# Performance work log

Measured on AMD Instinct MI355X. Metric: run time of the kernel, lower is better.

The kernel has to match this reference:

```python
import jax, jax.numpy as jnp
import numpy as np

N_NODES = 10000
N_EDGES = 320000
IN_DIM = 512
HID = 64
H0 = 8
OUT = 64
H1 = 1
NEG_SLOPE = 0.2


def gat_layer(h, src, dst, W, attn_l, attn_r, n_nodes, activation=None):
    # h: (N, F_in); W: (F_in, H*D); attn_l/attn_r: (H, D)
    H, D = attn_l.shape
    feat = (h @ W).reshape(n_nodes, H, D)            # (N, H, D)
    el = jnp.einsum('nhd,hd->nh', feat, attn_l)      # (N, H)
    er = jnp.einsum('nhd,hd->nh', feat, attn_r)      # (N, H)
    e = jax.nn.leaky_relu(el[src] + er[dst], NEG_SLOPE)  # (E, H)
    # edge softmax over incoming edges of each destination node
    m = jax.ops.segment_max(e, dst, num_segments=n_nodes)   # (N, H), -inf for isolated
    m = jnp.where(jnp.isfinite(m), m, 0.0)
    ex = jnp.exp(e - m[dst])                         # (E, H)
    s = jax.ops.segment_sum(ex, dst, num_segments=n_nodes)  # (N, H)
    alpha = ex / s[dst]                              # (E, H)
    # weighted aggregation: out[dst] += alpha * feat[src]
    out = jax.ops.segment_sum(alpha[:, :, None] * feat[src], dst,
                              num_segments=n_nodes)  # (N, H, D)
    if activation is not None:
        out = activation(out)
    return out


def setup_inputs() -> dict:
    key = jax.random.key(0)
    ks = jax.random.split(key, 9)
    h = jax.random.normal(ks[0], (N_NODES, IN_DIM), dtype=jnp.float32)
    src = jax.random.randint(ks[1], (N_EDGES,), 0, N_NODES, dtype=jnp.int32)
    dst = jax.random.randint(ks[2], (N_EDGES,), 0, N_NODES, dtype=jnp.int32)
    W1 = jax.random.normal(ks[3], (IN_DIM, H0 * HID), dtype=jnp.float32) / np.sqrt(IN_DIM)
    attn_l1 = jax.random.normal(ks[4], (H0, HID), dtype=jnp.float32) / np.sqrt(HID)
    attn_r1 = jax.random.normal(ks[5], (H0, HID), dtype=jnp.float32) / np.sqrt(HID)
    W2 = jax.random.normal(ks[6], (H0 * HID, H1 * OUT), dtype=jnp.float32) / np.sqrt(H0 * HID)
    attn_l2 = jax.random.normal(ks[7], (H1, OUT), dtype=jnp.float32) / np.sqrt(OUT)
    attn_r2 = jax.random.normal(ks[8], (H1, OUT), dtype=jnp.float32) / np.sqrt(OUT)
    return {"h": h, "src": src, "dst": dst, "W1": W1, "attn_l1": attn_l1,
            "attn_r1": attn_r1, "W2": W2, "attn_l2": attn_l2, "attn_r2": attn_r2}


def reference(h, src, dst, W1, attn_l1, attn_r1, W2, attn_l2, attn_r2):
    # layer 1: elu activation, concat heads (flatten)
    x = gat_layer(h, src, dst, W1, attn_l1, attn_r1, N_NODES, activation=jax.nn.elu)
    x = x.reshape(N_NODES, H0 * HID)
    # layer 2: no activation, mean over heads
    x = gat_layer(x, src, dst, W2, attn_l2, attn_r2, N_NODES, activation=None)
    return x.mean(axis=1)  # (N, OUT)
```

## Files before the change

kernel.cpp:

```cpp
#include <hip/hip_runtime.h>
#include <hip/hip_bf16.h>
#include <math.h>

typedef unsigned int u32;
typedef unsigned short ushort;

constexpr int N_NODES = 10000;
constexpr int N_EDGES = 320000;
constexpr float NEG_SLOPE = 0.2f;

typedef __attribute__((ext_vector_type(8))) _Float16 half8;
typedef __attribute__((ext_vector_type(4))) float f32x4;
typedef __attribute__((ext_vector_type(16))) float f32x16;

__device__ __forceinline__ float lrelu(float x) { return x > 0.f ? x : NEG_SLOPE * x; }
__device__ __forceinline__ float elu(float x)   { return x > 0.f ? x : (expf(x) - 1.f); }

__device__ __forceinline__ ushort f2h(float x) {
    _Float16 h = (_Float16)x;
    return __builtin_bit_cast(ushort, h);
}
__device__ __forceinline__ float h2f(ushort u) {
    return (float)__builtin_bit_cast(_Float16, u);
}

__device__ __forceinline__ void gload16(const void* g, void* l) {
    __builtin_amdgcn_global_load_lds(
        (__attribute__((address_space(1))) void*)g,
        (__attribute__((address_space(3))) void*)l, 16, 0, 0);
}

constexpr int NB_HIST  = (N_EDGES + 255) / 256;
constexpr int NB_SPLIT = (N_NODES * 512 / 4) / 256;

__global__ void prep1_kernel(const float4* __restrict__ h4,
                             ushort* __restrict__ xh,
                             const int* __restrict__ dst, int* __restrict__ counts,
                             int* __restrict__ rank) {
    const int b = blockIdx.x;
    if (b < NB_HIST) {
        const int i = b * 256 + threadIdx.x;
        if (i < N_EDGES) rank[i] = atomicAdd(&counts[dst[i]], 1);
    } else {
        const int i = (b - NB_HIST) * 256 + threadIdx.x;
        const float4 v = h4[i];
        *(ushort4*)&xh[i * 4] = make_ushort4(f2h(v.x), f2h(v.y), f2h(v.z), f2h(v.w));
    }
}

constexpr int NB_T1   = 64;
constexpr int NB_T2   = 8;
constexpr int NB_WLR2 = 2;

__global__ void prep2_kernel(const float* __restrict__ W1,
                             ushort* __restrict__ w1t,
                             const float* __restrict__ W2,
                             ushort* __restrict__ w2t,
                             const float* __restrict__ al2, const float* __restrict__ ar2,
                             float* __restrict__ wl2, float* __restrict__ wr2,
                             const int* __restrict__ counts, int* __restrict__ offs) {
    __shared__ float smem[64][65];
    const int b = blockIdx.x;
    if (b < NB_T1 + NB_T2) {
        const bool isW1 = b < NB_T1;
        const float* W = isW1 ? W1 : W2;
        ushort* wt = isW1 ? w1t : w2t;
        const int N  = isW1 ? 512 : 64;
        const int t  = isW1 ? b : (b - NB_T1);
        const int ti = isW1 ? (t & 7) : t;
        const int tj = isW1 ? (t >> 3) : 0;
        const int c  = threadIdx.x & 63;
        const int r0 = threadIdx.x >> 6;
#pragma unroll
        for (int p = 0; p < 16; p++) {
            const int r = p * 4 + r0;
            smem[r][c] = W[(size_t)(ti * 64 + r) * N + tj * 64 + c];
        }
        __syncthreads();
#pragma unroll
        for (int p = 0; p < 16; p++) {
            const int rr = p * 4 + r0;
            wt[(size_t)(tj * 64 + rr) * 512 + ti * 64 + c] = f2h(smem[c][rr]);
        }
    } else if (b < NB_T1 + NB_T2 + NB_WLR2) {
        const int k = (b - NB_T1 - NB_T2) * 256 + threadIdx.x;
        float sl = 0.f, sr = 0.f;
#pragma unroll 8
        for (int d = 0; d < 64; d++) {
            const float w = W2[(size_t)k * 64 + d];
            sl += w * al2[d];
            sr += w * ar2[d];
        }
        wl2[k] = sl;
        wr2[k] = sr;
    } else {
        __shared__ int wsum[4];
        const int tid = threadIdx.x;
        const int lane = tid & 63, wave = tid >> 6;
        const int base = tid * 40;
        int v[40];
        int s = 0;
#pragma unroll
        for (int i = 0; i < 40; i++) {
            v[i] = (base + i < N_NODES) ? counts[base + i] : 0;
            s += v[i];
        }
        int ps = s;
#pragma unroll
        for (int o = 1; o < 64; o <<= 1) {
            const int t = __shfl_up(ps, o);
            if (lane >= o) ps += t;
        }
        if (lane == 63) wsum[wave] = ps;
        __syncthreads();
        if (tid < 4) {
            int t = wsum[tid];
#pragma unroll
            for (int o = 1; o < 4; o <<= 1) {
                const int u = __shfl_up(t, o);
                if (tid >= o) t += u;
            }
            wsum[tid] = t;
        }
        __syncthreads();
        const int wbase = (wave > 0) ? wsum[wave - 1] : 0;
        int run = wbase + ps - s;
#pragma unroll
        for (int i = 0; i < 40; i++) {
            if (base + i < N_NODES) offs[base + i + 1] = run + v[i];
            run += v[i];
        }
        if (tid == 0) offs[0] = 0;
    }
}

constexpr int NB_GEMM1 = ((N_NODES + 63) / 64) * 4;
constexpr int NB_SCAT  = (N_EDGES + 255) / 256;

__global__ __launch_bounds__(256) void gemm1_scatter_kernel(
    const ushort* __restrict__ A, const ushort* __restrict__ B,
    ushort* __restrict__ Cout, int M,
    const float* __restrict__ attn_l, const float* __restrict__ attn_r,
    float* __restrict__ elp, float* __restrict__ erp,
    const int* __restrict__ src, const int* __restrict__ dst,
    const int* __restrict__ rank, const int* __restrict__ offs,
    int* __restrict__ srcs) {
    constexpr int BM = 64, BN = 128, BK = 32, K = 512, N = 512;

    if ((int)blockIdx.x >= NB_GEMM1) {
        const int i = ((int)blockIdx.x - NB_GEMM1) * 256 + threadIdx.x;
        if (i < N_EDGES) srcs[offs[dst[i]] + rank[i]] = src[i];
        return;
    }

    __shared__ __align__(16) ushort sA[BM * BK];
    __shared__ __align__(16) ushort sB[BN * BK];

    const int tid = threadIdx.x;
    const int wave = tid >> 6, lane = tid & 63;
    const int m0 = ((int)blockIdx.x >> 2) * BM, n0 = ((int)blockIdx.x & 3) * BN;
    const int wm = wave >> 1, wn = wave & 1;
    const int l31 = lane & 31, lh = lane >> 5;

    const int fb = wave * 1024 + lane * 16;

    int arow = m0 + (fb >> 6);
    if (arow > M - 1) arow = M - 1;
    const size_t abyte = (size_t)arow * (K * 2) + (fb & 63);
    size_t bbyte[2];
#pragma unroll
    for (int r = 0; r < 2; r++) {
        const int f = fb + r * 4096;
        bbyte[r] = (size_t)(n0 + (f >> 6)) * (K * 2) + (f & 63);
    }

    f32x16 acc[2] = {};

    for (int k0 = 0; k0 < K; k0 += BK) {
        __syncthreads();
        const size_t kb = (size_t)k0 * 2;
        gload16((const char*)A + abyte + kb, (char*)sA + fb);
#pragma unroll
        for (int r = 0; r < 2; r++) {
            const int f = fb + r * 4096;
            gload16((const char*)B + bbyte[r] + kb, (char*)sB + f);
        }
        __syncthreads();

#pragma unroll
        for (int ks = 0; ks < 2; ks++) {
            const int koff = ks * 16 + lh * 8;
            const half8 ah = *(const half8*)&sA[(wm * 32 + l31) * BK + koff];
#pragma unroll
            for (int ni = 0; ni < 2; ni++) {
                const half8 bh = *(const half8*)&sB[(wn * 64 + ni * 32 + l31) * BK + koff];
                acc[ni] = __builtin_amdgcn_mfma_f32_32x32x16_f16(ah, bh, acc[ni], 0, 0, 0);
            }
        }
    }

#pragma unroll
    for (int reg = 0; reg < 16; reg++) {
        const int grow = m0 + wm * 32 + (reg & 3) + 8 * (reg >> 2) + 4 * lh;
        if (grow < M) {
#pragma unroll
            for (int ni = 0; ni < 2; ni++) {
                const int gcol = n0 + wn * 64 + ni * 32 + l31;
                Cout[(size_t)grow * N + gcol] = f2h(acc[ni][reg]);
            }
        }
    }

    const int head = (n0 + wn * 64) >> 6;
    float alv[2], arv[2];
#pragma unroll
    for (int ni = 0; ni < 2; ni++) {
        alv[ni] = attn_l[head * 64 + ni * 32 + l31];
        arv[ni] = attn_r[head * 64 + ni * 32 + l31];
    }
#pragma unroll
    for (int reg = 0; reg < 16; reg++) {
        float pl = acc[0][reg] * alv[0] + acc[1][reg] * alv[1];
        float pr = acc[0][reg] * arv[0] + acc[1][reg] * arv[1];
#pragma unroll
        for (int o = 1; o < 32; o <<= 1) {
            pl += __shfl_xor(pl, o);
            pr += __shfl_xor(pr, o);
        }
        const int grow = m0 + wm * 32 + (reg & 3) + 8 * (reg >> 2) + 4 * lh;
        if (l31 == 0 && grow < M) {
            elp[grow * 8 + head] = pl;
            erp[grow * 8 + head] = pr;
        }
    }
}

__global__ __launch_bounds__(256) void gemm2_kernel(
    const ushort* __restrict__ A, const ushort* __restrict__ B,
    ushort* __restrict__ Cout, int M) {
    constexpr int BM = 64, BN = 64, BK = 32, K = 512, N = 64;
    constexpr int WM = 32, WN = 32, MT_M = 2, MT_N = 2;

    __shared__ __align__(16) ushort sA[BM * BK];
    __shared__ __align__(16) ushort sB[BN * BK];

    const int tid = threadIdx.x;
    const int wave = tid >> 6, lane = tid & 63;
    const int m0 = blockIdx.x * BM;
    const int wm = wave >> 1, wn = wave & 1;
    const int quad = lane >> 4, l15 = lane & 15;

    const int fb = wave * 1024 + lane * 16;

    int arow = m0 + (fb >> 6);
    if (arow > M - 1) arow = M - 1;
    const size_t abyte = (size_t)arow * (K * 2) + (fb & 63);
    const size_t bbyte = (size_t)(fb >> 6) * (K * 2) + (fb & 63);

    f32x4 acc[MT_M][MT_N] = {};

    for (int k0 = 0; k0 < K; k0 += BK) {
        __syncthreads();
        const size_t kb = (size_t)k0 * 2;
        gload16((const char*)A + abyte + kb, (char*)sA + fb);
        gload16((const char*)B + bbyte + kb, (char*)sB + fb);
        __syncthreads();

        half8 ah[MT_M], bh[MT_N];
#pragma unroll
        for (int mi = 0; mi < MT_M; mi++) {
            const int row = wm * WM + mi * 16 + l15;
            ah[mi] = *(const half8*)&sA[row * BK + quad * 8];
        }
#pragma unroll
        for (int ni = 0; ni < MT_N; ni++) {
            const int row = wn * WN + ni * 16 + l15;
            bh[ni] = *(const half8*)&sB[row * BK + quad * 8];
        }
#pragma unroll
        for (int mi = 0; mi < MT_M; mi++)
#pragma unroll
            for (int ni = 0; ni < MT_N; ni++)
                acc[mi][ni] = __builtin_amdgcn_mfma_f32_16x16x32_f16(ah[mi], bh[ni], acc[mi][ni], 0, 0, 0);
    }

#pragma unroll
    for (int mi = 0; mi < MT_M; mi++) {
#pragma unroll
        for (int r = 0; r < 4; r++) {
            const int grow = m0 + wm * WM + mi * 16 + quad * 4 + r;
            if (grow < M) {
#pragma unroll
                for (int ni = 0; ni < MT_N; ni++) {
                    const int gcol = wn * WN + ni * 16 + l15;
                    Cout[(size_t)grow * N + gcol] = f2h(acc[mi][ni][r]);
                }
            }
        }
    }
}

__global__ __launch_bounds__(256) void agg1_kernel(
    const ushort* __restrict__ feat, const float* __restrict__ el,
    const float* __restrict__ er, const int* __restrict__ offs,
    const int* __restrict__ srcs, ushort* __restrict__ xh,
    const float* __restrict__ wl2, const float* __restrict__ wr2,
    float* __restrict__ el2, float* __restrict__ er2) {
    const int tid = threadIdx.x;
    const int wave = tid >> 6, lane = tid & 63;
    const int node = blockIdx.x * 4 + wave;
    const int start = offs[node];
    const int deg = offs[node + 1] - start;
    const int d0 = lane * 8;
    const int myh = lane >> 3;

    if (deg == 0) {
        const ushort4 z = make_ushort4(0, 0, 0, 0);
        *(ushort4*)&xh[(size_t)node * 512 + d0] = z;
        *(ushort4*)&xh[(size_t)node * 512 + d0 + 4] = z;
        if (lane == 0) { el2[node] = 0.f; er2[node] = 0.f; }
        return;
    }

    const float4 ea = *(const float4*)&er[node * 8];
    const float4 eb = *(const float4*)&er[node * 8 + 4];
    const float er_my = (myh & 4) ? ((myh & 2) ? ((myh & 1) ? eb.w : eb.z)
                                              : ((myh & 1) ? eb.y : eb.x))
                                  : ((myh & 2) ? ((myh & 1) ? ea.w : ea.z)
                                              : ((myh & 1) ? ea.y : ea.x));

    float acc[8];
#pragma unroll
    for (int i = 0; i < 8; i++) acc[i] = 0.f;
    float ws = 0.f;

    for (int base = 0; base < deg; base += 64) {
        const int has = min(64, deg - base);
        const int s = srcs[start + base + min(lane, has - 1)];
        int j = 0;
        for (; j + 8 <= has; j += 8) {
            int sq[8];
#pragma unroll
            for (int q = 0; q < 8; q++) sq[q] = __shfl(s, j + q);
            float eq[8];
#pragma unroll
            for (int q = 0; q < 8; q++) eq[q] = el[sq[q] * 8 + myh];
            half8 uq[8];
#pragma unroll
            for (int q = 0; q < 8; q++)
                uq[q] = *(const half8*)&feat[(size_t)sq[q] * 512 + d0];
            float wq[8];
#pragma unroll
            for (int q = 0; q < 8; q++) wq[q] = __expf(lrelu(eq[q] + er_my));
#pragma unroll
            for (int q = 0; q < 8; q++) {
#pragma unroll
                for (int i = 0; i < 8; i++)
                    acc[i] += wq[q] * (float)uq[q][i];
                ws += wq[q];
            }
        }
        for (; j < has; j++) {
            const int sj = __shfl(s, j);
            const float w = __expf(lrelu(el[sj * 8 + myh] + er_my));
            const half8 u = *(const half8*)&feat[(size_t)sj * 512 + d0];
#pragma unroll
            for (int i = 0; i < 8; i++)
                acc[i] += w * (float)u[i];
            ws += w;
        }
    }

    const float inv = 1.f / ws;
    float o[8];
#pragma unroll
    for (int i = 0; i < 8; i++) o[i] = elu(acc[i] * inv);

    const float4 wla = *(const float4*)&wl2[d0];
    const float4 wlb = *(const float4*)&wl2[d0 + 4];
    const float4 wra = *(const float4*)&wr2[d0];
    const float4 wrb = *(const float4*)&wr2[d0 + 4];
    float pl = o[0] * wla.x + o[1] * wla.y + o[2] * wla.z + o[3] * wla.w
             + o[4] * wlb.x + o[5] * wlb.y + o[6] * wlb.z + o[7] * wlb.w;
    float pr = o[0] * wra.x + o[1] * wra.y + o[2] * wra.z + o[3] * wra.w
             + o[4] * wrb.x + o[5] * wrb.y + o[6] * wrb.z + o[7] * wrb.w;
#pragma unroll
    for (int off = 32; off > 0; off >>= 1) {
        pl += __shfl_xor(pl, off);
        pr += __shfl_xor(pr, off);
    }
    if (lane == 0) { el2[node] = pl; er2[node] = pr; }

    ushort hh[8];
#pragma unroll
    for (int i = 0; i < 8; i++) hh[i] = f2h(o[i]);
    *(ushort4*)&xh[(size_t)node * 512 + d0]     = make_ushort4(hh[0], hh[1], hh[2], hh[3]);
    *(ushort4*)&xh[(size_t)node * 512 + d0 + 4] = make_ushort4(hh[4], hh[5], hh[6], hh[7]);
}

__global__ __launch_bounds__(256) void agg2_kernel(
    const ushort* __restrict__ feat, const float* __restrict__ el,
    const float* __restrict__ er, const int* __restrict__ offs,
    const int* __restrict__ srcs, float* __restrict__ out) {
    const int tid = threadIdx.x;
    const int wave = tid >> 6, lane = tid & 63;
    const int node = blockIdx.x * 4 + wave;
    const int start = offs[node];
    const int deg = offs[node + 1] - start;
    if (deg == 0) { out[(size_t)node * 64 + lane] = 0.f; return; }
    const float ern = er[node];

    float acc = 0.f, ws = 0.f;
    for (int base = 0; base < deg; base += 64) {
        const int has = min(64, deg - base);
        const int s = srcs[start + base + min(lane, has - 1)];
        const float w = __expf(lrelu(el[s] + ern));
        int j = 0;
        for (; j + 8 <= has; j += 8) {
            float aq[8]; int sq[8];
#pragma unroll
            for (int q = 0; q < 8; q++) { aq[q] = __shfl(w, j + q); sq[q] = __shfl(s, j + q); }
            ushort fq[8];
#pragma unroll
            for (int q = 0; q < 8; q++) fq[q] = feat[(size_t)sq[q] * 64 + lane];
#pragma unroll
            for (int q = 0; q < 8; q++) { acc += aq[q] * h2f(fq[q]); ws += aq[q]; }
        }
        for (; j < has; j++) {
            const float a = __shfl(w, j);
            const int sj = __shfl(s, j);
            acc += a * h2f(feat[(size_t)sj * 64 + lane]);
            ws += a;
        }
    }
    out[(size_t)node * 64 + lane] = acc / ws;
}

extern "C" void kernel_launch(void* const* d_in, const int* in_sizes, int n_in,
                              void* d_out, int out_size, void* d_ws, size_t ws_size,
                              hipStream_t stream) {
    const float* h   = (const float*)d_in[0];
    const int*   src = (const int*)d_in[1];
    const int*   dst = (const int*)d_in[2];
    const float* W1  = (const float*)d_in[3];
    const float* al1 = (const float*)d_in[4];
    const float* ar1 = (const float*)d_in[5];
    const float* W2  = (const float*)d_in[6];
    const float* al2 = (const float*)d_in[7];
    const float* ar2 = (const float*)d_in[8];
    float* out = (float*)d_out;

    char* p = (char*)d_ws;
    ushort* feat1 = (ushort*)p; p += (size_t)N_NODES * 512 * 2;
    ushort* feat2 = (ushort*)p; p += (size_t)N_NODES * 64 * 2;
    float* el1   = (float*)p;  p += (size_t)N_NODES * 8 * 4;
    float* er1   = (float*)p;  p += (size_t)N_NODES * 8 * 4;
    float* el2   = (float*)p;  p += (size_t)N_NODES * 4;
    float* er2   = (float*)p;  p += (size_t)N_NODES * 4;
    ushort* xh   = (ushort*)p; p += (size_t)N_NODES * 512 * 2;
    ushort* w1t  = (ushort*)p; p += (size_t)512 * 512 * 2;
    ushort* w2t  = (ushort*)p; p += (size_t)64 * 512 * 2;
    float* wl2   = (float*)p;  p += (size_t)512 * 4;
    float* wr2   = (float*)p;  p += (size_t)512 * 4;
    int* counts  = (int*)p;    p += (size_t)N_NODES * 4;
    int* offs    = (int*)p;    p += (size_t)10004 * 4;
    int* rank    = (int*)p;    p += (size_t)N_EDGES * 4;
    int* srcs    = (int*)p;    p += (size_t)N_EDGES * 4;

    hipMemsetAsync(counts, 0, (size_t)N_NODES * 4, stream);

    prep1_kernel<<<NB_HIST + NB_SPLIT, 256, 0, stream>>>(
        (const float4*)h, xh, dst, counts, rank);

    prep2_kernel<<<NB_T1 + NB_T2 + NB_WLR2 + 1, 256, 0, stream>>>(
        W1, w1t, W2, w2t, al2, ar2, wl2, wr2, counts, offs);

    gemm1_scatter_kernel<<<NB_GEMM1 + NB_SCAT, 256, 0, stream>>>(
        xh, w1t, feat1, N_NODES, al1, ar1, el1, er1,
        src, dst, rank, offs, srcs);

    agg1_kernel<<<N_NODES / 4, 256, 0, stream>>>(
        feat1, el1, er1, offs, srcs, xh, wl2, wr2, el2, er2);

    gemm2_kernel<<<(N_NODES + 63) / 64, 256, 0, stream>>>(
        xh, w2t, feat2, N_NODES);

    agg2_kernel<<<N_NODES / 4, 256, 0, stream>>>(feat2, el2, er2, offs, srcs, out);
}
```

Before: 194.7 us.

## Double-buffer and swizzle LDS in both GEMMs, merge weight prep into first kernel

Both GEMM kernels now use BK=64 with double-buffered LDS tiles, prefetching the next k-tile via global_load_lds while computing the current one. An XOR swizzle on the LDS layout is meant to avoid bank conflicts. gemm2 halves BM to launch more blocks. The weight transpose and wl2/wr2 work moves into prep1 so that the single-block scan kernel runs alone, overlapping the prep work with the histogram and cast. The prefetch relies on the trailing __syncthreads per iteration to ensure the loads have completed.

```diff
diff --git a/kernel.cpp b/kernel.cpp
--- a/kernel.cpp
+++ b/kernel.cpp
@@ -31,42 +31,32 @@
 }
 
 constexpr int NB_HIST  = (N_EDGES + 255) / 256;
+constexpr int NB_T1    = 64;
+constexpr int NB_T2    = 8;
+constexpr int NB_WLR2  = 2;
+constexpr int NB_PRE   = NB_HIST + NB_T1 + NB_T2 + NB_WLR2;
 constexpr int NB_SPLIT = (N_NODES * 512 / 4) / 256;
 
 __global__ void prep1_kernel(const float4* __restrict__ h4,
                              ushort* __restrict__ xh,
                              const int* __restrict__ dst, int* __restrict__ counts,
-                             int* __restrict__ rank) {
+                             int* __restrict__ rank,
+                             const float* __restrict__ W1, ushort* __restrict__ w1t,
+                             const float* __restrict__ W2, ushort* __restrict__ w2t,
+                             const float* __restrict__ al2, const float* __restrict__ ar2,
+                             float* __restrict__ wl2, float* __restrict__ wr2) {
+    __shared__ float smem[64][65];
     const int b = blockIdx.x;
     if (b < NB_HIST) {
         const int i = b * 256 + threadIdx.x;
         if (i < N_EDGES) rank[i] = atomicAdd(&counts[dst[i]], 1);
-    } else {
-        const int i = (b - NB_HIST) * 256 + threadIdx.x;
-        const float4 v = h4[i];
-        *(ushort4*)&xh[i * 4] = make_ushort4(f2h(v.x), f2h(v.y), f2h(v.z), f2h(v.w));
-    }
-}
-
-constexpr int NB_T1   = 64;
-constexpr int NB_T2   = 8;
-constexpr int NB_WLR2 = 2;
-
-__global__ void prep2_kernel(const float* __restrict__ W1,
-                             ushort* __restrict__ w1t,
-                             const float* __restrict__ W2,
-                             ushort* __restrict__ w2t,
-                             const float* __restrict__ al2, const float* __restrict__ ar2,
-                             float* __restrict__ wl2, float* __restrict__ wr2,
-                             const int* __restrict__ counts, int* __restrict__ offs) {
-    __shared__ float smem[64][65];
-    const int b = blockIdx.x;
-    if (b < NB_T1 + NB_T2) {
-        const bool isW1 = b < NB_T1;
+    } else if (b < NB_HIST + NB_T1 + NB_T2) {
+        const int t0 = b - NB_HIST;
+        const bool isW1 = t0 < NB_T1;
         const float* W = isW1 ? W1 : W2;
         ushort* wt = isW1 ? w1t : w2t;
         const int N  = isW1 ? 512 : 64;
-        const int t  = isW1 ? b : (b - NB_T1);
+        const int t  = isW1 ? t0 : (t0 - NB_T1);
         const int ti = isW1 ? (t & 7) : t;
         const int tj = isW1 ? (t >> 3) : 0;
         const int c  = threadIdx.x & 63;
@@ -82,8 +72,8 @@
             const int rr = p * 4 + r0;
             wt[(size_t)(tj * 64 + rr) * 512 + ti * 64 + c] = f2h(smem[c][rr]);
         }
-    } else if (b < NB_T1 + NB_T2 + NB_WLR2) {
-        const int k = (b - NB_T1 - NB_T2) * 256 + threadIdx.x;
+    } else if (b < NB_PRE) {
+        const int k = (b - NB_HIST - NB_T1 - NB_T2) * 256 + threadIdx.x;
         float sl = 0.f, sr = 0.f;
 #pragma unroll 8
         for (int d = 0; d < 64; d++) {
@@ -94,44 +84,50 @@
         wl2[k] = sl;
         wr2[k] = sr;
     } else {
-        __shared__ int wsum[4];
-        const int tid = threadIdx.x;
-        const int lane = tid & 63, wave = tid >> 6;
-        const int base = tid * 40;
-        int v[40];
-        int s = 0;
-#pragma unroll
-        for (int i = 0; i < 40; i++) {
-            v[i] = (base + i < N_NODES) ? counts[base + i] : 0;
-            s += v[i];
-        }
-        int ps = s;
-#pragma unroll
-        for (int o = 1; o < 64; o <<= 1) {
-            const int t = __shfl_up(ps, o);
-            if (lane >= o) ps += t;
-        }
-        if (lane == 63) wsum[wave] = ps;
-        __syncthreads();
-        if (tid < 4) {
-            int t = wsum[tid];
-#pragma unroll
-            for (int o = 1; o < 4; o <<= 1) {
-                const int u = __shfl_up(t, o);
-                if (tid >= o) t += u;
-            }
-            wsum[tid] = t;
-        }
-        __syncthreads();
-        const int wbase = (wave > 0) ? wsum[wave - 1] : 0;
-        int run = wbase + ps - s;
-#pragma unroll
-        for (int i = 0; i < 40; i++) {
-            if (base + i < N_NODES) offs[base + i + 1] = run + v[i];
-            run += v[i];
-        }
-        if (tid == 0) offs[0] = 0;
-    }
+        const int i = (b - NB_PRE) * 256 + threadIdx.x;
+        const float4 v = h4[i];
+        *(ushort4*)&xh[i * 4] = make_ushort4(f2h(v.x), f2h(v.y), f2h(v.z), f2h(v.w));
+    }
+}
+
+__global__ void prep2_scan_kernel(const int* __restrict__ counts, int* __restrict__ offs) {
+    __shared__ int wsum[4];
+    const int tid = threadIdx.x;
+    const int lane = tid & 63, wave = tid >> 6;
+    const int base = tid * 40;
+    int v[40];
+    int s = 0;
+#pragma unroll
+    for (int i = 0; i < 40; i++) {
+        v[i] = (base + i < N_NODES) ? counts[base + i] : 0;
+        s += v[i];
+    }
+    int ps = s;
+#pragma unroll
+    for (int o = 1; o < 64; o <<= 1) {
+        const int t = __shfl_up(ps, o);
+        if (lane >= o) ps += t;
+    }
+    if (lane == 63) wsum[wave] = ps;
+    __syncthreads();
+    if (tid < 4) {
+        int t = wsum[tid];
+#pragma unroll
+        for (int o = 1; o < 4; o <<= 1) {
+            const int u = __shfl_up(t, o);
+            if (tid >= o) t += u;
+        }
+        wsum[tid] = t;
+    }
+    __syncthreads();
+    const int wbase = (wave > 0) ? wsum[wave - 1] : 0;
+    int run = wbase + ps - s;
+#pragma unroll
+    for (int i = 0; i < 40; i++) {
+        if (base + i < N_NODES) offs[base + i + 1] = run + v[i];
+        run += v[i];
+    }
+    if (tid == 0) offs[0] = 0;
 }
 
 constexpr int NB_GEMM1 = ((N_NODES + 63) / 64) * 4;
@@ -145,7 +141,7 @@
     const int* __restrict__ src, const int* __restrict__ dst,
     const int* __restrict__ rank, const int* __restrict__ offs,
     int* __restrict__ srcs) {
-    constexpr int BM = 64, BN = 128, BK = 32, K = 512, N = 512;
+    constexpr int BM = 64, BN = 128, BK = 64, K = 512, N = 512;
 
     if ((int)blockIdx.x >= NB_GEMM1) {
         const int i = ((int)blockIdx.x - NB_GEMM1) * 256 + threadIdx.x;
@@ -153,8 +149,8 @@
         return;
     }
 
-    __shared__ __align__(16) ushort sA[BM * BK];
-    __shared__ __align__(16) ushort sB[BN * BK];
+    __shared__ __align__(16) ushort sA[2][BM * BK];
+    __shared__ __align__(16) ushort sB[2][BN * BK];
 
     const int tid = threadIdx.x;
     const int wave = tid >> 6, lane = tid & 63;
@@ -162,41 +158,66 @@
     const int wm = wave >> 1, wn = wave & 1;
     const int l31 = lane & 31, lh = lane >> 5;
 
-    const int fb = wave * 1024 + lane * 16;
-
-    int arow = m0 + (fb >> 6);
-    if (arow > M - 1) arow = M - 1;
-    const size_t abyte = (size_t)arow * (K * 2) + (fb & 63);
-    size_t bbyte[2];
-#pragma unroll
-    for (int r = 0; r < 2; r++) {
-        const int f = fb + r * 4096;
-        bbyte[r] = (size_t)(n0 + (f >> 6)) * (K * 2) + (f & 63);
+    size_t abyte[2]; int afb[2];
+#pragma unroll
+    for (int p = 0; p < 2; p++) {
+        const int fb = tid * 16 + p * 4096;
+        const int r = fb >> 7, s = (fb >> 4) & 7;
+        int ar = m0 + r; if (ar > M - 1) ar = M - 1;
+        abyte[p] = (size_t)ar * (K * 2) + (size_t)((s ^ (r & 7)) << 4);
+        afb[p] = fb;
+    }
+    size_t bbyte[4]; int bfb[4];
+#pragma unroll
+    for (int p = 0; p < 4; p++) {
+        const int fb = tid * 16 + p * 4096;
+        const int r = fb >> 7, s = (fb >> 4) & 7;
+        bbyte[p] = (size_t)(n0 + r) * (K * 2) + (size_t)((s ^ (r & 7)) << 4);
+        bfb[p] = fb;
     }
 
     f32x16 acc[2] = {};
 
+    const int rA = wm * 32 + l31;
+    const u32 aoff = rA * 128, axr = rA & 7;
+    u32 boff[2], bxr[2];
+#pragma unroll
+    for (int ni = 0; ni < 2; ni++) {
+        const int rB = wn * 64 + ni * 32 + l31;
+        boff[ni] = rB * 128; bxr[ni] = rB & 7;
+    }
+
+#pragma unroll
+    for (int p = 0; p < 2; p++) gload16((const char*)A + abyte[p], (char*)&sA[0][0] + afb[p]);
+#pragma unroll
+    for (int p = 0; p < 4; p++) gload16((const char*)B + bbyte[p], (char*)&sB[0][0] + bfb[p]);
+    __syncthreads();
+
+    int cur = 0;
     for (int k0 = 0; k0 < K; k0 += BK) {
-        __syncthreads();
-        const size_t kb = (size_t)k0 * 2;
-        gload16((const char*)A + abyte + kb, (char*)sA + fb);
-#pragma unroll
-        for (int r = 0; r < 2; r++) {
-            const int f = fb + r * 4096;
-            gload16((const char*)B + bbyte[r] + kb, (char*)sB + f);
-        }
-        __syncthreads();
-
-#pragma unroll
-        for (int ks = 0; ks < 2; ks++) {
-            const int koff = ks * 16 + lh * 8;
-            const half8 ah = *(const half8*)&sA[(wm * 32 + l31) * BK + koff];
+        if (k0 + BK < K) {
+            const size_t kb = (size_t)(k0 + BK) * 2;
+#pragma unroll
+            for (int p = 0; p < 2; p++)
+                gload16((const char*)A + abyte[p] + kb, (char*)&sA[cur ^ 1][0] + afb[p]);
+#pragma unroll
+            for (int p = 0; p < 4; p++)
+                gload16((const char*)B + bbyte[p] + kb, (char*)&sB[cur ^ 1][0] + bfb[p]);
+        }
+        const char* pA = (const char*)&sA[cur][0];
+        const char* pB = (const char*)&sB[cur][0];
+#pragma unroll
+        for (int ks = 0; ks < 4; ks++) {
+            const u32 sl = ks * 2 + lh;
+            const half8 ah = *(const half8*)(pA + aoff + ((sl ^ axr) << 4));
 #pragma unroll
             for (int ni = 0; ni < 2; ni++) {
-                const half8 bh = *(const half8*)&sB[(wn * 64 + ni * 32 + l31) * BK + koff];
+                const half8 bh = *(const half8*)(pB + boff[ni] + ((sl ^ bxr[ni]) << 4));
                 acc[ni] = __builtin_amdgcn_mfma_f32_32x32x16_f16(ah, bh, acc[ni], 0, 0, 0);
             }
         }
+        __syncthreads();
+        cur ^= 1;
     }
 
 #pragma unroll
@@ -238,11 +259,10 @@
 __global__ __launch_bounds__(256) void gemm2_kernel(
     const ushort* __restrict__ A, const ushort* __restrict__ B,
     ushort* __restrict__ Cout, int M) {
-    constexpr int BM = 64, BN = 64, BK = 32, K = 512, N = 64;
-    constexpr int WM = 32, WN = 32, MT_M = 2, MT_N = 2;
-
-    __shared__ __align__(16) ushort sA[BM * BK];
-    __shared__ __align__(16) ushort sB[BN * BK];
+    constexpr int BM = 32, BN = 64, BK = 64, K = 512, N = 64;
+
+    __shared__ __align__(16) ushort sA[2][BM * BK];
+    __shared__ __align__(16) ushort sB[2][BN * BK];
 
     const int tid = threadIdx.x;
     const int wave = tid >> 6, lane = tid & 63;
@@ -250,51 +270,68 @@
     const int wm = wave >> 1, wn = wave & 1;
     const int quad = lane >> 4, l15 = lane & 15;
 
-    const int fb = wave * 1024 + lane * 16;
-
-    int arow = m0 + (fb >> 6);
-    if (arow > M - 1) arow = M - 1;
-    const size_t abyte = (size_t)arow * (K * 2) + (fb & 63);
-    const size_t bbyte = (size_t)(fb >> 6) * (K * 2) + (fb & 63);
-
-    f32x4 acc[MT_M][MT_N] = {};
-
+    const int fa = tid * 16;
+    const int ra = fa >> 7, sa_ = (fa >> 4) & 7;
+    int arow = m0 + ra; if (arow > M - 1) arow = M - 1;
+    const size_t abyte = (size_t)arow * (K * 2) + (size_t)((sa_ ^ (ra & 7)) << 4);
+
+    size_t bbyte[2]; int bfb[2];
+#pragma unroll
+    for (int p = 0; p < 2; p++) {
+        const int fb = tid * 16 + p * 4096;
+        const int r = fb >> 7, s = (fb >> 4) & 7;
+        bbyte[p] = (size_t)r * (K * 2) + (size_t)((s ^ (r & 7)) << 4);
+        bfb[p] = fb;
+    }
+
+    f32x4 acc[2] = {};
+    const int rA = wm * 16 + l15;
+    const u32 aoff = rA * 128, axr = rA & 7;
+    u32 boff[2], bxr[2];
+#pragma unroll
+    for (int ni = 0; ni < 2; ni++) {
+        const int rB = wn * 32 + ni * 16 + l15;
+        boff[ni] = rB * 128; bxr[ni] = rB & 7;
+    }
+
+    gload16((const char*)A + abyte, (char*)&sA[0][0] + fa);
+#pragma unroll
+    for (int p = 0; p < 2; p++) gload16((const char*)B + bbyte[p], (char*)&sB[0][0] + bfb[p]);
+    __syncthreads();
+
+    int cur = 0;
     for (int k0 = 0; k0 < K; k0 += BK) {
+        if (k0 + BK < K) {
+            const size_t kb = (size_t)(k0 + BK) * 2;
+            gload16((const char*)A + abyte + kb, (char*)&sA[cur ^ 1][0] + fa);
+#pragma unroll
+            for (int p = 0; p < 2; p++)
+                gload16((const char*)B + bbyte[p] + kb, (char*)&sB[cur ^ 1][0] + bfb[p]);
+        }
+        const char* pA = (const char*)&sA[cur][0];
+        const char* pB = (const char*)&sB[cur][0];
+#pragma unroll
+        for (int ks = 0; ks < 2; ks++) {
+            const u32 sl = ks * 4 + quad;
+            const half8 ah = *(const half8*)(pA + aoff + ((sl ^ axr) << 4));
+#pragma unroll
+            for (int ni = 0; ni < 2; ni++) {
+                const half8 bh = *(const half8*)(pB + boff[ni] + ((sl ^ bxr[ni]) << 4));
+                acc[ni] = __builtin_amdgcn_mfma_f32_16x16x32_f16(ah, bh, acc[ni], 0, 0, 0);
+            }
+        }
         __syncthreads();
-        const size_t kb = (size_t)k0 * 2;
-        gload16((const char*)A + abyte + kb, (char*)sA + fb);
-        gload16((const char*)B + bbyte + kb, (char*)sB + fb);
-        __syncthreads();
-
-        half8 ah[MT_M], bh[MT_N];
-#pragma unroll
-        for (int mi = 0; mi < MT_M; mi++) {
-            const int row = wm * WM + mi * 16 + l15;
-            ah[mi] = *(const half8*)&sA[row * BK + quad * 8];
-        }
-#pragma unroll
-        for (int ni = 0; ni < MT_N; ni++) {
-            const int row = wn * WN + ni * 16 + l15;
-            bh[ni] = *(const half8*)&sB[row * BK + quad * 8];
-        }
-#pragma unroll
-        for (int mi = 0; mi < MT_M; mi++)
-#pragma unroll
-            for (int ni = 0; ni < MT_N; ni++)
-                acc[mi][ni] = __builtin_amdgcn_mfma_f32_16x16x32_f16(ah[mi], bh[ni], acc[mi][ni], 0, 0, 0);
-    }
-
-#pragma unroll
-    for (int mi = 0; mi < MT_M; mi++) {
-#pragma unroll
-        for (int r = 0; r < 4; r++) {
-            const int grow = m0 + wm * WM + mi * 16 + quad * 4 + r;
-            if (grow < M) {
-#pragma unroll
-                for (int ni = 0; ni < MT_N; ni++) {
-                    const int gcol = wn * WN + ni * 16 + l15;
-                    Cout[(size_t)grow * N + gcol] = f2h(acc[mi][ni][r]);
-                }
+        cur ^= 1;
+    }
+
+#pragma unroll
+    for (int r = 0; r < 4; r++) {
+        const int grow = m0 + wm * 16 + quad * 4 + r;
+        if (grow < M) {
+#pragma unroll
+            for (int ni = 0; ni < 2; ni++) {
+                const int gcol = wn * 32 + ni * 16 + l15;
+                Cout[(size_t)grow * N + gcol] = f2h(acc[ni][r]);
             }
         }
     }
@@ -469,11 +506,11 @@
 
     hipMemsetAsync(counts, 0, (size_t)N_NODES * 4, stream);
 
-    prep1_kernel<<<NB_HIST + NB_SPLIT, 256, 0, stream>>>(
-        (const float4*)h, xh, dst, counts, rank);
-
-    prep2_kernel<<<NB_T1 + NB_T2 + NB_WLR2 + 1, 256, 0, stream>>>(
-        W1, w1t, W2, w2t, al2, ar2, wl2, wr2, counts, offs);
+    prep1_kernel<<<NB_PRE + NB_SPLIT, 256, 0, stream>>>(
+        (const float4*)h, xh, dst, counts, rank,
+        W1, w1t, W2, w2t, al2, ar2, wl2, wr2);
+
+    prep2_scan_kernel<<<1, 256, 0, stream>>>(counts, offs);
 
     gemm1_scatter_kernel<<<NB_GEMM1 + NB_SCAT, 256, 0, stream>>>(
         xh, w1t, feat1, N_NODES, al1, ar1, el1, er1,
@@ -482,7 +519,7 @@
     agg1_kernel<<<N_NODES / 4, 256, 0, stream>>>(
         feat1, el1, er1, offs, srcs, xh, wl2, wr2, el2, er2);
 
-    gemm2_kernel<<<(N_NODES + 63) / 64, 256, 0, stream>>>(
+    gemm2_kernel<<<(N_NODES + 31) / 32, 256, 0, stream>>>(
         xh, w2t, feat2, N_NODES);
 
     agg2_kernel<<<N_NODES / 4, 256, 0, stream>>>(feat2, el2, er2, offs, srcs, out);
```

Result: no change. 194.4 us (-0.2%).
